# Optimization experiments

Measured on AMD Instinct MI355X. Metric: run time of the kernel, lower is better.

The kernel has to match this reference:

```python
import jax, jax.numpy as jnp
import numpy as np

B, LP, NC, D, E = 8, 1000, 64, 128, 320  # batch, protein len, compound atoms, hid dim, esm dim


def _linear_params(key, din, dout):
    k1, k2 = jax.random.split(key)
    lim = 1.0 / np.sqrt(din)
    W = jax.random.uniform(k1, (din, dout), minval=-lim, maxval=lim, dtype=jnp.float32)
    b = jax.random.uniform(k2, (dout,), minval=-lim, maxval=lim, dtype=jnp.float32)
    return W, b


def setup_inputs() -> dict:
    key = jax.random.key(0)
    ks = jax.random.split(key, 14)
    inp = {
        "protein_embedding": jax.random.normal(ks[0], (B, LP, E), dtype=jnp.float32),
        "protein_feat_x": jax.random.normal(ks[1], (B, LP, D), dtype=jnp.float32),
        "compound_feats": jax.random.normal(ks[2], (B, NC, D), dtype=jnp.float32),
    }
    layers = [("emb", E, D), ("wq", D, D), ("wk", D, D), ("wv", D, D), ("wo", D, D),
              ("jp", D, D), ("jc", D, D),
              ("c1", D, 1024), ("c2", 1024, 1024), ("c3", 1024, 256), ("c4", 256, 1)]
    for i, (name, din, dout) in enumerate(layers):
        W, b = _linear_params(ks[3 + i], din, dout)
        inp[name + "_w"] = W
        inp[name + "_b"] = b
    return inp


def reference(protein_embedding, protein_feat_x, compound_feats,
              emb_w, emb_b, wq_w, wq_b, wk_w, wk_b, wv_w, wv_b, wo_w, wo_b,
              jp_w, jp_b, jc_w, jc_b,
              c1_w, c1_b, c2_w, c2_b, c3_w, c3_b, c4_w, c4_b):
    # protein sequence embedding -> hid dim
    pe = protein_embedding @ emb_w + emb_b                      # [B, LP, D]
    # single-head cross attention: query = seq embedding, key/value = graph feats
    Q = pe @ wq_w + wq_b
    K = protein_feat_x @ wk_w + wk_b
    V = protein_feat_x @ wv_w + wv_b
    scale = jnp.sqrt(jnp.asarray(D, pe.dtype))                  # n_heads=1 -> head_dim=D
    attn = jax.nn.softmax(jnp.einsum('bqd,bkd->bqk', Q, K) / scale, axis=-1)
    protein_feats = jnp.einsum('bqk,bkd->bqd', attn, V) @ wo_w + wo_b  # [B, LP, D]

    # sigmoid bilinear joint attention over (protein residue, compound atom) pairs
    P = jax.nn.relu(protein_feats) @ jp_w + jp_b                # [B, LP, D]
    C = jax.nn.relu(compound_feats) @ jc_w + jc_b               # [B, NC, D]
    A = jax.nn.sigmoid(jnp.einsum('bid,bkd->bik', P, C))        # [B, LP, NC]
    A = A / jnp.sum(A, axis=(1, 2), keepdims=True)

    # tanh outer product (the costly 4D bikj intermediate) then weighted reduction
    cp = jnp.tanh(protein_feats[:, :, None, :] * compound_feats[:, None, :, :])  # [B, LP, NC, D]
    cp_embedding = jnp.einsum('bikd,bik->bd', cp, A)            # [B, D]

    # classifier MLP (dropout is eval-mode identity)
    h = jax.nn.relu(cp_embedding @ c1_w + c1_b)
    h = jax.nn.relu(h @ c2_w + c2_b)
    h = jax.nn.relu(h @ c3_w + c3_b)
    return h @ c4_w + c4_b                                      # [B, 1]
```

## Files before the change

kernel.cpp:

```cpp
#include <hip/hip_runtime.h>
#include <hip/hip_bf16.h>
#include <math.h>

#define LP 1000
#define NCMP 64
#define NSPLIT 4

typedef _Float16 f16;
typedef f16   v8h __attribute__((ext_vector_type(8)));
typedef float v4f __attribute__((ext_vector_type(4)));

__device__ __forceinline__ float rcp_fast(float x) { return __builtin_amdgcn_rcpf(x); }
__device__ __forceinline__ void fsplit(float x, f16& h, f16& l) {
    h = (f16)x; l = (f16)(x - (float)h);
}

__device__ __forceinline__ void gemm_core(float (*Ws)[128], float (*Xt)[36],
                                          const float* X, const float* W, const float* bias,
                                          float* Y, int K, int rowbase, bool relu_in)
{
    const int t  = threadIdx.x;
    const int r0 = (t >> 5) * 4;
    const int c0 = (t & 31) * 4;
    const int xr = t >> 3, xk = (t & 7) << 2;
    const int xrow = rowbase + xr;
    float4 xv = *(const float4*)(X + (long)xrow * K + xk);
    float4 wv[4];
    #pragma unroll
    for (int u = 0; u < 4; ++u) {
        int s = t + u * 256, r = s >> 5, cb = (s & 31) << 2;
        wv[u] = *(const float4*)(W + (long)r * 128 + cb);
    }
    float acc[4][4] = {};
    for (int k0 = 0; k0 < K; k0 += 32) {
        float4 xs = xv;
        if (relu_in) { xs.x = fmaxf(xs.x,0.f); xs.y = fmaxf(xs.y,0.f);
                       xs.z = fmaxf(xs.z,0.f); xs.w = fmaxf(xs.w,0.f); }
        Xt[xk+0][xr] = xs.x; Xt[xk+1][xr] = xs.y; Xt[xk+2][xr] = xs.z; Xt[xk+3][xr] = xs.w;
        #pragma unroll
        for (int u = 0; u < 4; ++u) {
            int s = t + u * 256, r = s >> 5, cb = (s & 31) << 2;
            *(float4*)&Ws[r][cb] = wv[u];
        }
        __syncthreads();
        if (k0 + 32 < K) {
            xv = *(const float4*)(X + (long)xrow * K + k0 + 32 + xk);
            #pragma unroll
            for (int u = 0; u < 4; ++u) {
                int s = t + u * 256, r = s >> 5, cb = (s & 31) << 2;
                wv[u] = *(const float4*)(W + (long)(k0 + 32 + r) * 128 + cb);
            }
        }
        #pragma unroll
        for (int kk = 0; kk < 32; ++kk) {
            float4 w4 = *(const float4*)&Ws[kk][c0];
            float4 x4 = *(const float4*)&Xt[kk][r0];
            acc[0][0] = fmaf(x4.x, w4.x, acc[0][0]); acc[0][1] = fmaf(x4.x, w4.y, acc[0][1]);
            acc[0][2] = fmaf(x4.x, w4.z, acc[0][2]); acc[0][3] = fmaf(x4.x, w4.w, acc[0][3]);
            acc[1][0] = fmaf(x4.y, w4.x, acc[1][0]); acc[1][1] = fmaf(x4.y, w4.y, acc[1][1]);
            acc[1][2] = fmaf(x4.y, w4.z, acc[1][2]); acc[1][3] = fmaf(x4.y, w4.w, acc[1][3]);
            acc[2][0] = fmaf(x4.z, w4.x, acc[2][0]); acc[2][1] = fmaf(x4.z, w4.y, acc[2][1]);
            acc[2][2] = fmaf(x4.z, w4.z, acc[2][2]); acc[2][3] = fmaf(x4.z, w4.w, acc[2][3]);
            acc[3][0] = fmaf(x4.w, w4.x, acc[3][0]); acc[3][1] = fmaf(x4.w, w4.y, acc[3][1]);
            acc[3][2] = fmaf(x4.w, w4.z, acc[3][2]); acc[3][3] = fmaf(x4.w, w4.w, acc[3][3]);
        }
        __syncthreads();
    }
    float4 bv = bias ? *(const float4*)(bias + c0) : make_float4(0.f,0.f,0.f,0.f);
    #pragma unroll
    for (int i = 0; i < 4; ++i) {
        int row = rowbase + r0 + i;
        float4 o;
        o.x = acc[i][0] + bv.x; o.y = acc[i][1] + bv.y;
        o.z = acc[i][2] + bv.z; o.w = acc[i][3] + bv.w;
        *(float4*)(Y + (long)row * 128 + c0) = o;
    }
}

struct H4 { f16 a, b, c, d; };

__device__ __forceinline__ void gemm_core16(float (*Ws)[128], float (*Xt)[36],
                                            const float* X, const float* W, const float* bias,
                                            f16* Yhi, f16* Ylo, int K, int rowbase)
{
    const int t  = threadIdx.x;
    const int r0 = (t >> 5) * 4;
    const int c0 = (t & 31) * 4;
    const int xr = t >> 3, xk = (t & 7) << 2;
    const int xrow = rowbase + xr;
    float4 xv = *(const float4*)(X + (long)xrow * K + xk);
    float4 wv[4];
    #pragma unroll
    for (int u = 0; u < 4; ++u) {
        int s = t + u * 256, r = s >> 5, cb = (s & 31) << 2;
        wv[u] = *(const float4*)(W + (long)r * 128 + cb);
    }
    float acc[4][4] = {};
    for (int k0 = 0; k0 < K; k0 += 32) {
        Xt[xk+0][xr] = xv.x; Xt[xk+1][xr] = xv.y; Xt[xk+2][xr] = xv.z; Xt[xk+3][xr] = xv.w;
        #pragma unroll
        for (int u = 0; u < 4; ++u) {
            int s = t + u * 256, r = s >> 5, cb = (s & 31) << 2;
            *(float4*)&Ws[r][cb] = wv[u];
        }
        __syncthreads();
        if (k0 + 32 < K) {
            xv = *(const float4*)(X + (long)xrow * K + k0 + 32 + xk);
            #pragma unroll
            for (int u = 0; u < 4; ++u) {
                int s = t + u * 256, r = s >> 5, cb = (s & 31) << 2;
                wv[u] = *(const float4*)(W + (long)(k0 + 32 + r) * 128 + cb);
            }
        }
        #pragma unroll
        for (int kk = 0; kk < 32; ++kk) {
            float4 w4 = *(const float4*)&Ws[kk][c0];
            float4 x4 = *(const float4*)&Xt[kk][r0];
            acc[0][0] = fmaf(x4.x, w4.x, acc[0][0]); acc[0][1] = fmaf(x4.x, w4.y, acc[0][1]);
            acc[0][2] = fmaf(x4.x, w4.z, acc[0][2]); acc[0][3] = fmaf(x4.x, w4.w, acc[0][3]);
            acc[1][0] = fmaf(x4.y, w4.x, acc[1][0]); acc[1][1] = fmaf(x4.y, w4.y, acc[1][1]);
            acc[1][2] = fmaf(x4.y, w4.z, acc[1][2]); acc[1][3] = fmaf(x4.y, w4.w, acc[1][3]);
            acc[2][0] = fmaf(x4.z, w4.x, acc[2][0]); acc[2][1] = fmaf(x4.z, w4.y, acc[2][1]);
            acc[2][2] = fmaf(x4.z, w4.z, acc[2][2]); acc[2][3] = fmaf(x4.z, w4.w, acc[2][3]);
            acc[3][0] = fmaf(x4.w, w4.x, acc[3][0]); acc[3][1] = fmaf(x4.w, w4.y, acc[3][1]);
            acc[3][2] = fmaf(x4.w, w4.z, acc[3][2]); acc[3][3] = fmaf(x4.w, w4.w, acc[3][3]);
        }
        __syncthreads();
    }
    float4 bv = *(const float4*)(bias + c0);
    #pragma unroll
    for (int i = 0; i < 4; ++i) {
        int row = rowbase + r0 + i;
        int bb = row / 1000, rr = row - bb * 1000;
        long base = ((long)bb * 1024 + rr) * 128 + c0;
        float o0 = acc[i][0]+bv.x, o1 = acc[i][1]+bv.y, o2 = acc[i][2]+bv.z, o3 = acc[i][3]+bv.w;
        H4 h, l;
        fsplit(o0, h.a, l.a); fsplit(o1, h.b, l.b); fsplit(o2, h.c, l.c); fsplit(o3, h.d, l.d);
        *(H4*)(Yhi + base) = h;
        *(H4*)(Ylo + base) = l;
    }
}

__global__ __launch_bounds__(256) void pre0_k(const float* __restrict__ emb_w, const float* __restrict__ emb_b,
                                              const float* __restrict__ wq_w, const float* __restrict__ wq_b,
                                              const float* __restrict__ wv_w, const float* __restrict__ wv_b,
                                              const float* __restrict__ wo_w, const float* __restrict__ wo_b,
                                              float* __restrict__ Wp, float* __restrict__ bp,
                                              float* __restrict__ Wvo, float* __restrict__ bvo,
                                              float* __restrict__ zbase)
{
    __shared__ __align__(16) float Ws[32][128];
    __shared__ __align__(16) float Xt[32][36];
    const int bid = blockIdx.x;
    if (bid < 10) { gemm_core(Ws, Xt, emb_w, wq_w, nullptr, Wp, 128, bid * 32, false); return; }
    if (bid >= 11 && bid < 15) { gemm_core(Ws, Xt, wv_w, wo_w, nullptr, Wvo, 128, (bid - 11) * 32, false); return; }
    int t = threadIdx.x;
    if (bid == 10 && t >= 128) {
        for (int i = t - 128; i < 1032; i += 128) zbase[i] = 0.f;
        return;
    }
    if (t < 128) {
        const float* vb = (bid == 10) ? emb_b : wv_b;
        const float* Wm = (bid == 10) ? wq_w  : wo_w;
        const float* ab = (bid == 10) ? wq_b  : wo_b;
        float a0 = 0.f, a1 = 0.f, a2 = 0.f, a3 = 0.f;
        for (int k = 0; k < 128; k += 4) {
            a0 = fmaf(vb[k+0], Wm[(k+0)*128 + t], a0);
            a1 = fmaf(vb[k+1], Wm[(k+1)*128 + t], a1);
            a2 = fmaf(vb[k+2], Wm[(k+2)*128 + t], a2);
            a3 = fmaf(vb[k+3], Wm[(k+3)*128 + t], a3);
        }
        float* dst = (bid == 10) ? bp : bvo;
        dst[t] = (a0 + a1) + (a2 + a3) + ab[t];
    }
}

__global__ __launch_bounds__(256) void qkv_k(const float* __restrict__ PE, const float* __restrict__ Wp,
                                             const float* __restrict__ bp, const float* __restrict__ PFX,
                                             const float* __restrict__ wk_w, const float* __restrict__ wk_b,
                                             const float* __restrict__ CF, const float* __restrict__ jc_w,
                                             const float* __restrict__ jc_b,
                                             f16* __restrict__ Qhi, f16* __restrict__ Qlo,
                                             f16* __restrict__ Khi, f16* __restrict__ Klo,
                                             f16* __restrict__ Vthi, f16* __restrict__ Vtlo,
                                             float* __restrict__ Cj)
{
    __shared__ __align__(16) float Ws[32][128];
    __shared__ __align__(16) float Xt[32][36];
    const int bid = blockIdx.x;
    if (bid < 250) { gemm_core16(Ws, Xt, PE, Wp, bp, Qhi, Qlo, 320, bid * 32); return; }
    if (bid < 500) { gemm_core16(Ws, Xt, PFX, wk_w, wk_b, Khi, Klo, 128, (bid - 250) * 32); return; }
    if (bid < 516) { gemm_core(Ws, Xt, CF, jc_w, jc_b, Cj, 128, (bid - 500) * 32, true); return; }
    const int t = threadIdx.x;
    const int rowbase = (bid - 516) * 32;
    const int d = t >> 1, half = t & 1;
    #pragma unroll 4
    for (int i = 0; i < 16; ++i) {
        int row = rowbase + half * 16 + i;
        int bb = row / 1000, rr = row - bb * 1000;
        float v = PFX[(long)row * 128 + d];
        f16 h, l; fsplit(v, h, l);
        long o = ((long)bb * 128 + d) * 1024 + rr;
        Vthi[o] = h; Vtlo[o] = l;
    }
}

__global__ __launch_bounds__(256) void flash7_k(const f16* __restrict__ Qhi, const f16* __restrict__ Qlo,
                                                const f16* __restrict__ Khi, const f16* __restrict__ Klo,
                                                const f16* __restrict__ Vthi, const f16* __restrict__ Vtlo,
                                                float* __restrict__ Opart,
                                                float* __restrict__ mpart, float* __restrict__ lpart)
{
    __shared__ __align__(16) f16 KVhi[9216];
    __shared__ __align__(16) f16 KVlo[9216];
    __shared__ __align__(16) f16 Pshi[4][16 * 72];
    __shared__ __align__(16) f16 Pslo[4][16 * 72];
    const int t    = threadIdx.x;
    const int wv   = t >> 6;
    const int lane = t & 63;
    const int quad = lane >> 4;
    const int l4   = lane & 15;
    const int qt = blockIdx.x, sp = blockIdx.y, b = blockIdx.z;
    const int q0 = qt * 64;
    const float SCALE = 0.08838834764831845f;
    const float L2E   = 1.4426950408889634f;

    int qrow = q0 + wv * 16 + l4; if (qrow >= LP) qrow = LP - 1;
    const long qbase = ((long)b * 1024 + qrow) * 128;
    v8h qh[4], ql[4];
    #pragma unroll
    for (int kt4 = 0; kt4 < 4; ++kt4) {
        qh[kt4] = *(const v8h*)(Qhi + qbase + kt4 * 32 + quad * 8);
        ql[kt4] = *(const v8h*)(Qlo + qbase + kt4 * 32 + quad * 8);
    }
    float m_i[4] = { -3.0e38f, -3.0e38f, -3.0e38f, -3.0e38f };
    float l_i[4] = { 0.f, 0.f, 0.f, 0.f };
    v4f  O[8];
    #pragma unroll
    for (int dt = 0; dt < 8; ++dt) O[dt] = (v4f){0.f, 0.f, 0.f, 0.f};

    for (int kt = sp * 4; kt < sp * 4 + 4; ++kt) {
        const int key0 = kt * 64;
        __syncthreads();
        #pragma unroll
        for (int u = 0; u < 4; ++u) {
            int ch = t + u * 256;
            int r = ch >> 4, co = (ch & 15) * 8;
            long ga = ((long)b * 1024 + key0 + r) * 128 + co;
            *(v8h*)(KVhi + r * 136 + co) = *(const v8h*)(Khi + ga);
            *(v8h*)(KVlo + r * 136 + co) = *(const v8h*)(Klo + ga);
        }
        __syncthreads();
        v8h vh[4], vl[4];
        #pragma unroll
        for (int u = 0; u < 4; ++u) {
            int ch = t + u * 256;
            int d = ch >> 3, co = (ch & 7) * 8;
            long ga = ((long)b * 128 + d) * 1024 + key0 + co;
            vh[u] = *(const v8h*)(Vthi + ga);
            vl[u] = *(const v8h*)(Vtlo + ga);
        }
        v4f S[4];
        #pragma unroll
        for (int nt = 0; nt < 4; ++nt) S[nt] = (v4f){0.f, 0.f, 0.f, 0.f};
        #pragma unroll
        for (int nt = 0; nt < 4; ++nt) {
            const int rb = (nt * 16 + l4) * 136;
            #pragma unroll
            for (int kt4 = 0; kt4 < 4; ++kt4) {
                v8h bh = *(const v8h*)(KVhi + rb + kt4 * 32 + quad * 8);
                v8h bl = *(const v8h*)(KVlo + rb + kt4 * 32 + quad * 8);
                S[nt] = __builtin_amdgcn_mfma_f32_16x16x32_f16(qh[kt4], bh, S[nt], 0, 0, 0);
                S[nt] = __builtin_amdgcn_mfma_f32_16x16x32_f16(qh[kt4], bl, S[nt], 0, 0, 0);
                S[nt] = __builtin_amdgcn_mfma_f32_16x16x32_f16(ql[kt4], bh, S[nt], 0, 0, 0);
            }
        }
        #pragma unroll
        for (int nt = 0; nt < 4; ++nt) {
            bool valid = (key0 + nt * 16 + l4) < LP;
            #pragma unroll
            for (int r = 0; r < 4; ++r)
                S[nt][r] = valid ? S[nt][r] * SCALE : -3.0e38f;
        }
        float alpha[4];
        #pragma unroll
        for (int r = 0; r < 4; ++r) {
            float tm = fmaxf(fmaxf(S[0][r], S[1][r]), fmaxf(S[2][r], S[3][r]));
            tm = fmaxf(tm, __shfl_xor(tm, 1));
            tm = fmaxf(tm, __shfl_xor(tm, 2));
            tm = fmaxf(tm, __shfl_xor(tm, 4));
            tm = fmaxf(tm, __shfl_xor(tm, 8));
            float mnew = fmaxf(m_i[r], tm);
            alpha[r] = exp2f((m_i[r] - mnew) * L2E);
            float ps = 0.f;
            #pragma unroll
            for (int nt = 0; nt < 4; ++nt) {
                float p = exp2f((S[nt][r] - mnew) * L2E);
                S[nt][r] = p;
                ps += p;
            }
            ps += __shfl_xor(ps, 1);
            ps += __shfl_xor(ps, 2);
            ps += __shfl_xor(ps, 4);
            ps += __shfl_xor(ps, 8);
            l_i[r] = l_i[r] * alpha[r] + ps;
            m_i[r] = mnew;
        }
        #pragma unroll
        for (int dt = 0; dt < 8; ++dt) {
            O[dt][0] *= alpha[0]; O[dt][1] *= alpha[1];
            O[dt][2] *= alpha[2]; O[dt][3] *= alpha[3];
        }
        __syncthreads();
        #pragma unroll
        for (int u = 0; u < 4; ++u) {
            int ch = t + u * 256;
            int d = ch >> 3, co = (ch & 7) * 8;
            *(v8h*)(KVhi + d * 72 + co) = vh[u];
            *(v8h*)(KVlo + d * 72 + co) = vl[u];
        }
        #pragma unroll
        for (int nt = 0; nt < 4; ++nt) {
            int col = nt * 16 + l4;
            #pragma unroll
            for (int r = 0; r < 4; ++r) {
                f16 ph, pl; fsplit(S[nt][r], ph, pl);
                Pshi[wv][(quad * 4 + r) * 72 + col] = ph;
                Pslo[wv][(quad * 4 + r) * 72 + col] = pl;
            }
        }
        __syncthreads();
        #pragma unroll
        for (int kc = 0; kc < 2; ++kc) {
            v8h pah = *(const v8h*)(Pshi[wv] + l4 * 72 + kc * 32 + quad * 8);
            v8h pal = *(const v8h*)(Pslo[wv] + l4 * 72 + kc * 32 + quad * 8);
            #pragma unroll
            for (int dt = 0; dt < 8; ++dt) {
                v8h vfh = *(const v8h*)(KVhi + (dt * 16 + l4) * 72 + kc * 32 + quad * 8);
                v8h vfl = *(const v8h*)(KVlo + (dt * 16 + l4) * 72 + kc * 32 + quad * 8);
                O[dt] = __builtin_amdgcn_mfma_f32_16x16x32_f16(pah, vfh, O[dt], 0, 0, 0);
                O[dt] = __builtin_amdgcn_mfma_f32_16x16x32_f16(pah, vfl, O[dt], 0, 0, 0);
                O[dt] = __builtin_amdgcn_mfma_f32_16x16x32_f16(pal, vfh, O[dt], 0, 0, 0);
            }
        }
    }
    #pragma unroll
    for (int r = 0; r < 4; ++r) {
        int row = q0 + wv * 16 + quad * 4 + r;
        if (row < LP) {
            long base = (long)sp * 1024000 + ((long)b * LP + row) * 128;
            #pragma unroll
            for (int dt = 0; dt < 8; ++dt)
                Opart[base + dt * 16 + l4] = O[dt][r];
            if (l4 == 0) {
                mpart[(long)sp * 8000 + b * LP + row] = m_i[r];
                lpart[(long)sp * 8000 + b * LP + row] = l_i[r];
            }
        }
    }
}

__global__ __launch_bounds__(256) void megatail_k(
    const float* __restrict__ Opart, const float* __restrict__ mp, const float* __restrict__ lp,
    const float* __restrict__ Wvo, const float* __restrict__ bvo,
    const float* __restrict__ jp_w, const float* __restrict__ jp_b,
    const float* __restrict__ Cj, const float* __restrict__ CF,
    float* __restrict__ Asum, float* __restrict__ cpe)
{
    __shared__ __align__(16) float WsA[32][132];
    __shared__ __align__(16) float Xt[32][20];
    __shared__ __align__(16) float AttS[16][132];
    __shared__ __align__(16) float Csh[64][132];
    __shared__ __align__(16) float Ash[16][64];
    __shared__ __align__(16) float AshT[64][20];
    __shared__ float red[256];
    const int t = threadIdx.x;
    const int p0 = blockIdx.x * 16;
    const int b  = blockIdx.y;
    const float L2E = 1.4426950408889634f;

    #pragma unroll
    for (int u = 0; u < 8; ++u) {
        int s = t + u * 256, r = s >> 5, cb = (s & 31) << 2;
        *(float4*)&Csh[r][cb] = *(const float4*)(Cj + ((long)b * NCMP + r) * 128 + cb);
    }
    const int r0 = (t >> 5) * 2, c0 = (t & 31) * 4;
    const int xr = t >> 3, xk = (t & 7) << 2;
    int prow = p0 + xr; if (prow > LP - 1) prow = LP - 1;
    const long g = (long)b * LP + prow;
    float wgt[NSPLIT]; float linv = 0.f;
    if (t < 128) {
        float mm = -3.0e38f;
        #pragma unroll
        for (int s = 0; s < NSPLIT; ++s) mm = fmaxf(mm, mp[g + (long)s * 8000]);
        float ls = 0.f;
        #pragma unroll
        for (int s = 0; s < NSPLIT; ++s) {
            wgt[s] = exp2f((mp[g + (long)s * 8000] - mm) * L2E);
            ls += wgt[s] * lp[g + (long)s * 8000];
        }
        linv = 1.0f / ls;
    }
    float4 xv = make_float4(0.f,0.f,0.f,0.f);
    float4 wv[4];
    if (t < 128) {
        float4 a = make_float4(0.f,0.f,0.f,0.f);
        #pragma unroll
        for (int s = 0; s < NSPLIT; ++s) {
            float4 p = *(const float4*)(Opart + (long)s * 1024000 + g * 128 + xk);
            a.x = fmaf(wgt[s], p.x, a.x); a.y = fmaf(wgt[s], p.y, a.y);
            a.z = fmaf(wgt[s], p.z, a.z); a.w = fmaf(wgt[s], p.w, a.w);
        }
        xv = make_float4(a.x * linv, a.y * linv, a.z * linv, a.w * linv);
    }
    #pragma unroll
    for (int u = 0; u < 4; ++u) {
        int s = t + u * 256, r = s >> 5, cb = (s & 31) << 2;
        wv[u] = *(const float4*)(Wvo + (long)r * 128 + cb);
    }
    float acc[2][4] = {};
    for (int k0 = 0; k0 < 128; k0 += 32) {
        if (t < 128) { Xt[xk+0][xr]=xv.x; Xt[xk+1][xr]=xv.y; Xt[xk+2][xr]=xv.z; Xt[xk+3][xr]=xv.w; }
        #pragma unroll
        for (int u = 0; u < 4; ++u) {
            int s = t + u * 256, r = s >> 5, cb = (s & 31) << 2;
            *(float4*)&WsA[r][cb] = wv[u];
        }
        __syncthreads();
        if (k0 + 32 < 128) {
            int kn = k0 + 32;
            if (t < 128) {
                float4 a = make_float4(0.f,0.f,0.f,0.f);
                #pragma unroll
                for (int s = 0; s < NSPLIT; ++s) {
                    float4 p = *(const float4*)(Opart + (long)s * 1024000 + g * 128 + kn + xk);
                    a.x = fmaf(wgt[s], p.x, a.x); a.y = fmaf(wgt[s], p.y, a.y);
                    a.z = fmaf(wgt[s], p.z, a.z); a.w = fmaf(wgt[s], p.w, a.w);
                }
                xv = make_float4(a.x * linv, a.y * linv, a.z * linv, a.w * linv);
            }
            #pragma unroll
            for (int u = 0; u < 4; ++u) {
                int s = t + u * 256, r = s >> 5, cb = (s & 31) << 2;
                wv[u] = *(const float4*)(Wvo + (long)(kn + r) * 128 + cb);
            }
        }
        #pragma unroll
        for (int kk = 0; kk < 32; ++kk) {
            float2 x2 = *(const float2*)&Xt[kk][r0];
            float4 w4 = *(const float4*)&WsA[kk][c0];
            acc[0][0]=fmaf(x2.x,w4.x,acc[0][0]); acc[0][1]=fmaf(x2.x,w4.y,acc[0][1]);
            acc[0][2]=fmaf(x2.x,w4.z,acc[0][2]); acc[0][3]=fmaf(x2.x,w4.w,acc[0][3]);
            acc[1][0]=fmaf(x2.y,w4.x,acc[1][0]); acc[1][1]=fmaf(x2.y,w4.y,acc[1][1]);
            acc[1][2]=fmaf(x2.y,w4.z,acc[1][2]); acc[1][3]=fmaf(x2.y,w4.w,acc[1][3]);
        }
        __syncthreads();
    }
    {
        float4 bv1 = *(const float4*)(bvo + c0);
        #pragma unroll
        for (int i = 0; i < 2; ++i)
            *(float4*)&AttS[r0 + i][c0] =
                make_float4(acc[i][0]+bv1.x, acc[i][1]+bv1.y, acc[i][2]+bv1.z, acc[i][3]+bv1.w);
    }
    float4 wv2[4];
    #pragma unroll
    for (int u = 0; u < 4; ++u) {
        int s = t + u * 256, r = s >> 5, cb = (s & 31) << 2;
        wv2[u] = *(const float4*)(jp_w + (long)r * 128 + cb);
    }
    float ac2[2][4] = {};
    for (int k0 = 0; k0 < 128; k0 += 32) {
        #pragma unroll
        for (int u = 0; u < 4; ++u) {
            int s = t + u * 256, r = s >> 5, cb = (s & 31) << 2;
            *(float4*)&WsA[r][cb] = wv2[u];
        }
        __syncthreads();
        if (k0 + 32 < 128) {
            #pragma unroll
            for (int u = 0; u < 4; ++u) {
                int s = t + u * 256, r = s >> 5, cb = (s & 31) << 2;
                wv2[u] = *(const float4*)(jp_w + (long)(k0 + 32 + r) * 128 + cb);
            }
        }
        #pragma unroll
        for (int kq = 0; kq < 8; ++kq) {
            float4 xa = *(const float4*)&AttS[r0 + 0][k0 + (kq << 2)];
            float4 xb = *(const float4*)&AttS[r0 + 1][k0 + (kq << 2)];
            #pragma unroll
            for (int e = 0; e < 4; ++e) {
                float x0 = fmaxf((e==0)?xa.x:(e==1)?xa.y:(e==2)?xa.z:xa.w, 0.f);
                float x1 = fmaxf((e==0)?xb.x:(e==1)?xb.y:(e==2)?xb.z:xb.w, 0.f);
                float4 w4 = *(const float4*)&WsA[(kq << 2) + e][c0];
                ac2[0][0]=fmaf(x0,w4.x,ac2[0][0]); ac2[0][1]=fmaf(x0,w4.y,ac2[0][1]);
                ac2[0][2]=fmaf(x0,w4.z,ac2[0][2]); ac2[0][3]=fmaf(x0,w4.w,ac2[0][3]);
                ac2[1][0]=fmaf(x1,w4.x,ac2[1][0]); ac2[1][1]=fmaf(x1,w4.y,ac2[1][1]);
                ac2[1][2]=fmaf(x1,w4.z,ac2[1][2]); ac2[1][3]=fmaf(x1,w4.w,ac2[1][3]);
            }
        }
        __syncthreads();
    }
    float (*Psh)[132] = WsA;
    {
        float4 b2 = *(const float4*)(jp_b + c0);
        #pragma unroll
        for (int i = 0; i < 2; ++i)
            *(float4*)&Psh[r0 + i][c0] =
                make_float4(ac2[i][0]+b2.x, ac2[i][1]+b2.y, ac2[i][2]+b2.z, ac2[i][3]+b2.w);
    }
    __syncthreads();
    const int tr = t >> 4, tc = t & 15;
    float sacc[4] = {};
    #pragma unroll 4
    for (int d4 = 0; d4 < 32; ++d4) {
        float4 p4 = *(const float4*)&Psh[tr][d4 << 2];
        #pragma unroll
        for (int j = 0; j < 4; ++j) {
            float4 cv = *(const float4*)&Csh[tc + (j << 4)][d4 << 2];
            sacc[j] += p4.x*cv.x + p4.y*cv.y + p4.z*cv.z + p4.w*cv.w;
        }
    }
    float lsum = 0.f;
    {
        int gi = p0 + tr;
        #pragma unroll
        for (int j = 0; j < 4; ++j) {
            float sg = rcp_fast(1.f + exp2f(-sacc[j] * L2E));
            if (gi < LP) {
                Ash[tr][tc + (j << 4)]  = sg;
                AshT[tc + (j << 4)][tr] = sg;
                lsum += sg;
            }
        }
    }
    red[t] = lsum;
    __syncthreads();
    for (int off = 128; off > 0; off >>= 1) {
        if (t < off) red[t] += red[t + off];
        __syncthreads();
    }
    if (t == 0) atomicAdd(Asum + b, red[0]);
    __syncthreads();
    #pragma unroll
    for (int u = 0; u < 8; ++u) {
        int s = t + u * 256, r = s >> 5, cb = (s & 31) << 2;
        *(float4*)&Csh[r][cb] = *(const float4*)(CF + ((long)b * NCMP + r) * 128 + cb);
    }
    __syncthreads();
    const float TWO_L2E = 2.8853900817779268f;
    const int d  = t & 127;
    const int kh = t >> 7;
    const int iiN = (LP - p0 < 16) ? (LP - p0) : 16;
    float areg[16];
    #pragma unroll
    for (int ii = 0; ii < 16; ++ii) areg[ii] = AttS[ii][d] * TWO_L2E;
    float accD = 0.f;
    for (int kk = 0; kk < 32; ++kk) {
        const int k = (kh << 5) + kk;
        const float cv = Csh[k][d];
        for (int iq = 0; iq < iiN; iq += 4) {
            float4 a4 = *(const float4*)&AshT[k][iq];
            float e0 = exp2f(areg[iq+0] * cv);
            float e1 = exp2f(areg[iq+1] * cv);
            float e2 = exp2f(areg[iq+2] * cv);
            float e3 = exp2f(areg[iq+3] * cv);
            accD = fmaf(1.f - 2.f * rcp_fast(e0 + 1.f), a4.x, accD);
            accD = fmaf(1.f - 2.f * rcp_fast(e1 + 1.f), a4.y, accD);
            accD = fmaf(1.f - 2.f * rcp_fast(e2 + 1.f), a4.z, accD);
            accD = fmaf(1.f - 2.f * rcp_fast(e3 + 1.f), a4.w, accD);
        }
    }
    red[t] = accD;
    __syncthreads();
    if (t < 128) atomicAdd(cpe + (long)b * 128 + t, red[t] + red[t + 128]);
}

__global__ __launch_bounds__(256) void c12_k(const float* __restrict__ cpe, const float* __restrict__ Asum,
                                             const float* __restrict__ c1_w, const float* __restrict__ c1_b,
                                             const float* __restrict__ c2_w, float* __restrict__ part)
{
    __shared__ float sc[8][128];
    __shared__ float ins[8][8];
    const int t = threadIdx.x, ks = blockIdx.x, k0 = ks * 8;
    #pragma unroll
    for (int u = 0; u < 4; ++u) {
        int idx = t + u * 256;
        sc[idx >> 7][idx & 127] = cpe[idx] * rcp_fast(Asum[idx >> 7]);
    }
    __syncthreads();
    if (t < 64) {
        int b = t >> 3, kk = t & 7;
        int n1 = k0 + kk;
        float a0 = 0.f, a1 = 0.f, a2 = 0.f, a3 = 0.f;
        #pragma unroll 8
        for (int j = 0; j < 128; j += 4) {
            a0 = fmaf(sc[b][j+0], c1_w[(long)(j+0)*1024 + n1], a0);
            a1 = fmaf(sc[b][j+1], c1_w[(long)(j+1)*1024 + n1], a1);
            a2 = fmaf(sc[b][j+2], c1_w[(long)(j+2)*1024 + n1], a2);
            a3 = fmaf(sc[b][j+3], c1_w[(long)(j+3)*1024 + n1], a3);
        }
        ins[b][kk] = fmaxf((a0 + a1) + (a2 + a3) + c1_b[n1], 0.f);
    }
    __syncthreads();
    const int n = (t & 63) * 4 + (t >> 6) * 256;
    float4 acc[8] = {};
    #pragma unroll
    for (int kk = 0; kk < 8; ++kk) {
        float4 w4 = *(const float4*)(c2_w + (long)(k0 + kk) * 1024 + n);
        #pragma unroll
        for (int b = 0; b < 8; ++b) {
            float s = ins[b][kk];
            acc[b].x = fmaf(s, w4.x, acc[b].x); acc[b].y = fmaf(s, w4.y, acc[b].y);
            acc[b].z = fmaf(s, w4.z, acc[b].z); acc[b].w = fmaf(s, w4.w, acc[b].w);
        }
    }
    #pragma unroll
    for (int b = 0; b < 8; ++b)
        *(float4*)(part + ((long)(ks * 8 + b)) * 1024 + n) = acc[b];
}

__global__ __launch_bounds__(256) void c3m_k(const float* __restrict__ part2, const float* __restrict__ c2_b,
                                             const float* __restrict__ c3_w, const float* __restrict__ c3_b,
                                             const float* __restrict__ c4_w, const float* __restrict__ c4_b,
                                             float* __restrict__ out)
{
    __shared__ float Hs[1024];
    __shared__ float red[256];
    const int t = threadIdx.x, b = blockIdx.x;
    float4 acc4 = make_float4(0.f,0.f,0.f,0.f);
    #pragma unroll 4
    for (int ks = 0; ks < 128; ++ks) {
        float4 p = *(const float4*)(part2 + ((long)(ks * 8 + b)) * 1024 + t * 4);
        acc4.x += p.x; acc4.y += p.y; acc4.z += p.z; acc4.w += p.w;
    }
    {
        float4 bb = *(const float4*)(c2_b + t * 4);
        Hs[t*4+0] = fmaxf(acc4.x + bb.x, 0.f);
        Hs[t*4+1] = fmaxf(acc4.y + bb.y, 0.f);
        Hs[t*4+2] = fmaxf(acc4.z + bb.z, 0.f);
        Hs[t*4+3] = fmaxf(acc4.w + bb.w, 0.f);
    }
    __syncthreads();
    float a0 = 0.f, a1 = 0.f, a2 = 0.f, a3 = 0.f;
    #pragma unroll 8
    for (int k = 0; k < 1024; k += 4) {
        a0 = fmaf(Hs[k+0], c3_w[(long)(k+0)*256 + t], a0);
        a1 = fmaf(Hs[k+1], c3_w[(long)(k+1)*256 + t], a1);
        a2 = fmaf(Hs[k+2], c3_w[(long)(k+2)*256 + t], a2);
        a3 = fmaf(Hs[k+3], c3_w[(long)(k+3)*256 + t], a3);
    }
    float h3v = fmaxf((a0 + a1) + (a2 + a3) + c3_b[t], 0.f);
    red[t] = h3v * c4_w[t];
    __syncthreads();
    for (int off = 128; off > 0; off >>= 1) {
        if (t < off) red[t] += red[t + off];
        __syncthreads();
    }
    if (t == 0) out[b] = red[0] + c4_b[0];
}

extern "C" void kernel_launch(void* const* d_in, const int* in_sizes, int n_in,
                              void* d_out, int out_size, void* d_ws, size_t ws_size,
                              hipStream_t stream)
{
    const float* PE   = (const float*)d_in[0];
    const float* PFX  = (const float*)d_in[1];
    const float* CF   = (const float*)d_in[2];
    const float* emb_w = (const float*)d_in[3];  const float* emb_b = (const float*)d_in[4];
    const float* wq_w  = (const float*)d_in[5];  const float* wq_b  = (const float*)d_in[6];
    const float* wk_w  = (const float*)d_in[7];  const float* wk_b  = (const float*)d_in[8];
    const float* wv_w  = (const float*)d_in[9];  const float* wv_b  = (const float*)d_in[10];
    const float* wo_w  = (const float*)d_in[11]; const float* wo_b  = (const float*)d_in[12];
    const float* jp_w  = (const float*)d_in[13]; const float* jp_b  = (const float*)d_in[14];
    const float* jc_w  = (const float*)d_in[15]; const float* jc_b  = (const float*)d_in[16];
    const float* c1_w  = (const float*)d_in[17]; const float* c1_b  = (const float*)d_in[18];
    const float* c2_w  = (const float*)d_in[19]; const float* c2_b  = (const float*)d_in[20];
    const float* c3_w  = (const float*)d_in[21]; const float* c3_b  = (const float*)d_in[22];
    const float* c4_w  = (const float*)d_in[23]; const float* c4_b  = (const float*)d_in[24];

    float* ws     = (float*)d_ws;
    f16*  Qhi   = (f16*)ws;
    f16*  Qlo   = (f16*)(ws + 524288);
    f16*  Khi   = (f16*)(ws + 1048576);
    f16*  Klo   = (f16*)(ws + 1572864);
    f16*  Vthi  = (f16*)(ws + 2097152);
    f16*  Vtlo  = (f16*)(ws + 2621440);
    float* bufC   = ws + 3145728;
    float* Opart  = bufC + 65536;
    float* mpart  = Opart + 4096000;
    float* lpart  = mpart + 32000;
    float* Asum   = lpart + 32000;
    float* cpe    = Asum + 8;
    float* bprime = cpe + 1024;
    float* bufWp  = bprime + 128;
    float* bufWvo = bufWp + 40960;
    float* bufbvo = bufWvo + 16384;
    float* part2  = ws;

    pre0_k<<<16, 256, 0, stream>>>(emb_w, emb_b, wq_w, wq_b, wv_w, wv_b, wo_w, wo_b,
                                   bufWp, bprime, bufWvo, bufbvo, Asum);
    qkv_k<<<766, 256, 0, stream>>>(PE, bufWp, bprime, PFX, wk_w, wk_b, CF, jc_w, jc_b,
                                   Qhi, Qlo, Khi, Klo, Vthi, Vtlo, bufC);
    flash7_k<<<dim3(16, NSPLIT, 8), 256, 0, stream>>>(Qhi, Qlo, Khi, Klo, Vthi, Vtlo,
                                                      Opart, mpart, lpart);
    megatail_k<<<dim3(63, 8), 256, 0, stream>>>(Opart, mpart, lpart, bufWvo, bufbvo,
                                                jp_w, jp_b, bufC, CF, Asum, cpe);
    c12_k<<<128, 256, 0, stream>>>(cpe, Asum, c1_w, c1_b, c2_w, part2);
    c3m_k<<<8, 256, 0, stream>>>(part2, c2_b, c3_w, c3_b, c4_w, c4_b, (float*)d_out);
}
```

Measured before the change: 278.8 us.

## Split megatail into projection kernel and compound-chunked tanh reduction kernel

```diff
diff --git a/kernel.cpp b/kernel.cpp
--- a/kernel.cpp
+++ b/kernel.cpp
@@ -360,30 +360,20 @@
     }
 }
 
-__global__ __launch_bounds__(256) void megatail_k(
+__global__ __launch_bounds__(256) void mt1_k(
     const float* __restrict__ Opart, const float* __restrict__ mp, const float* __restrict__ lp,
     const float* __restrict__ Wvo, const float* __restrict__ bvo,
     const float* __restrict__ jp_w, const float* __restrict__ jp_b,
-    const float* __restrict__ Cj, const float* __restrict__ CF,
-    float* __restrict__ Asum, float* __restrict__ cpe)
+    float* __restrict__ PF, float* __restrict__ PJ)
 {
     __shared__ __align__(16) float WsA[32][132];
     __shared__ __align__(16) float Xt[32][20];
     __shared__ __align__(16) float AttS[16][132];
-    __shared__ __align__(16) float Csh[64][132];
-    __shared__ __align__(16) float Ash[16][64];
-    __shared__ __align__(16) float AshT[64][20];
-    __shared__ float red[256];
     const int t = threadIdx.x;
     const int p0 = blockIdx.x * 16;
     const int b  = blockIdx.y;
     const float L2E = 1.4426950408889634f;
 
-    #pragma unroll
-    for (int u = 0; u < 8; ++u) {
-        int s = t + u * 256, r = s >> 5, cb = (s & 31) << 2;
-        *(float4*)&Csh[r][cb] = *(const float4*)(Cj + ((long)b * NCMP + r) * 128 + cb);
-    }
     const int r0 = (t >> 5) * 2, c0 = (t & 31) * 4;
     const int xr = t >> 3, xk = (t & 7) << 2;
     int prow = p0 + xr; if (prow > LP - 1) prow = LP - 1;
@@ -459,9 +449,12 @@
     {
         float4 bv1 = *(const float4*)(bvo + c0);
         #pragma unroll
-        for (int i = 0; i < 2; ++i)
-            *(float4*)&AttS[r0 + i][c0] =
-                make_float4(acc[i][0]+bv1.x, acc[i][1]+bv1.y, acc[i][2]+bv1.z, acc[i][3]+bv1.w);
+        for (int i = 0; i < 2; ++i) {
+            float4 o = make_float4(acc[i][0]+bv1.x, acc[i][1]+bv1.y, acc[i][2]+bv1.z, acc[i][3]+bv1.w);
+            *(float4*)&AttS[r0 + i][c0] = o;
+            int row = p0 + r0 + i;
+            if (row < LP) *(float4*)(PF + ((long)b * LP + row) * 128 + c0) = o;
+        }
     }
     float4 wv2[4];
     #pragma unroll
@@ -501,65 +494,28 @@
         }
         __syncthreads();
     }
-    float (*Psh)[132] = WsA;
     {
         float4 b2 = *(const float4*)(jp_b + c0);
         #pragma unroll
-        for (int i = 0; i < 2; ++i)
-            *(float4*)&Psh[r0 + i][c0] =
-                make_float4(ac2[i][0]+b2.x, ac2[i][1]+b2.y, ac2[i][2]+b2.z, ac2[i][3]+b2.w);
-    }
-    __syncthreads();
-    const int tr = t >> 4, tc = t & 15;
-    float sacc[4] = {};
-    #pragma unroll 4
-    for (int d4 = 0; d4 < 32; ++d4) {
-        float4 p4 = *(const float4*)&Psh[tr][d4 << 2];
-        #pragma unroll
-        for (int j = 0; j < 4; ++j) {
-            float4 cv = *(const float4*)&Csh[tc + (j << 4)][d4 << 2];
-            sacc[j] += p4.x*cv.x + p4.y*cv.y + p4.z*cv.z + p4.w*cv.w;
-        }
-    }
-    float lsum = 0.f;
-    {
-        int gi = p0 + tr;
-        #pragma unroll
-        for (int j = 0; j < 4; ++j) {
-            float sg = rcp_fast(1.f + exp2f(-sacc[j] * L2E));
-            if (gi < LP) {
-                Ash[tr][tc + (j << 4)]  = sg;
-                AshT[tc + (j << 4)][tr] = sg;
-                lsum += sg;
-            }
-        }
-    }
-    red[t] = lsum;
-    __syncthreads();
-    for (int off = 128; off > 0; off >>= 1) {
-        if (t < off) red[t] += red[t + off];
-        __syncthreads();
-    }
-    if (t == 0) atomicAdd(Asum + b, red[0]);
-    __syncthreads();
-    #pragma unroll
-    for (int u = 0; u < 8; ++u) {
-        int s = t + u * 256, r = s >> 5, cb = (s & 31) << 2;
-        *(float4*)&Csh[r][cb] = *(const float4*)(CF + ((long)b * NCMP + r) * 128 + cb);
-    }
-    __syncthreads();
-    const float TWO_L2E = 2.8853900817779268f;
-    const int d  = t & 127;
-    const int kh = t >> 7;
-    const int iiN = (LP - p0 < 16) ? (LP - p0) : 16;
-    float areg[16];
-    #pragma unroll
-    for (int ii = 0; ii < 16; ++ii) areg[ii] = AttS[ii][d] * TWO_L2E;
+        for (int i = 0; i < 2; ++i) {
+            int row = p0 + r0 + i;
+            if (row < LP)
+                *(float4*)(PJ + ((long)b * LP + row) * 128 + c0) =
+                    make_float4(ac2[i][0]+b2.x, ac2[i][1]+b2.y, ac2[i][2]+b2.z, ac2[i][3]+b2.w);
+        }
+    }
+}
+
+template<int IIN>
+__device__ __forceinline__ float tanh_chunk(const float (*Cs)[132], const float (*AshT)[20],
+                                            const float* areg, int d, int kh)
+{
     float accD = 0.f;
-    for (int kk = 0; kk < 32; ++kk) {
-        const int k = (kh << 5) + kk;
-        const float cv = Csh[k][d];
-        for (int iq = 0; iq < iiN; iq += 4) {
+    for (int kk = 0; kk < 16; ++kk) {
+        const int k = (kh << 4) + kk;
+        const float cv = Cs[k][d];
+        #pragma unroll
+        for (int iq = 0; iq < IIN; iq += 4) {
             float4 a4 = *(const float4*)&AshT[k][iq];
             float e0 = exp2f(areg[iq+0] * cv);
             float e1 = exp2f(areg[iq+1] * cv);
@@ -571,6 +527,78 @@
             accD = fmaf(1.f - 2.f * rcp_fast(e3 + 1.f), a4.w, accD);
         }
     }
+    return accD;
+}
+
+__global__ __launch_bounds__(256) void mt2_k(
+    const float* __restrict__ PF, const float* __restrict__ PJ,
+    const float* __restrict__ Cj, const float* __restrict__ CF,
+    float* __restrict__ Asum, float* __restrict__ cpe)
+{
+    __shared__ __align__(16) float Pjs[16][132];
+    __shared__ __align__(16) float Pfs[16][132];
+    __shared__ __align__(16) float Cs[32][132];
+    __shared__ __align__(16) float AshT[32][20];
+    __shared__ float red[256];
+    const int t  = threadIdx.x;
+    const int p0 = blockIdx.x * 16;
+    const int kc = blockIdx.y;
+    const int b  = blockIdx.z;
+    const float L2E = 1.4426950408889634f;
+
+    {
+        int pr = t >> 4, pc = (t & 15) << 3;
+        int gr = p0 + pr; if (gr > LP - 1) gr = LP - 1;
+        long gb = ((long)b * LP + gr) * 128 + pc;
+        *(float4*)&Pjs[pr][pc]     = *(const float4*)(PJ + gb);
+        *(float4*)&Pjs[pr][pc + 4] = *(const float4*)(PJ + gb + 4);
+        *(float4*)&Pfs[pr][pc]     = *(const float4*)(PF + gb);
+        *(float4*)&Pfs[pr][pc + 4] = *(const float4*)(PF + gb + 4);
+    }
+    float4 cfv[4];
+    #pragma unroll
+    for (int u = 0; u < 4; ++u) {
+        int s = t + u * 256, r = s >> 5, cb = (s & 31) << 2;
+        *(float4*)&Cs[r][cb] = *(const float4*)(Cj + ((long)b * NCMP + kc * 32 + r) * 128 + cb);
+        cfv[u] = *(const float4*)(CF + ((long)b * NCMP + kc * 32 + r) * 128 + cb);
+    }
+    __syncthreads();
+    const int tr = t >> 4, tc = t & 15;
+    float sacc[2] = {0.f, 0.f};
+    #pragma unroll 4
+    for (int d4 = 0; d4 < 32; ++d4) {
+        float4 p4 = *(const float4*)&Pjs[tr][d4 << 2];
+        #pragma unroll
+        for (int j = 0; j < 2; ++j) {
+            float4 cv = *(const float4*)&Cs[tc + (j << 4)][d4 << 2];
+            sacc[j] += p4.x*cv.x + p4.y*cv.y + p4.z*cv.z + p4.w*cv.w;
+        }
+    }
+    float lsum = 0.f;
+    const int gi = p0 + tr;
+    #pragma unroll
+    for (int j = 0; j < 2; ++j) {
+        float sg = rcp_fast(1.f + exp2f(-sacc[j] * L2E));
+        if (gi < LP) { AshT[tc + (j << 4)][tr] = sg; lsum += sg; }
+    }
+    #pragma unroll
+    for (int off = 1; off < 64; off <<= 1) lsum += __shfl_xor(lsum, off);
+    if ((t & 63) == 0) red[t >> 6] = lsum;
+    __syncthreads();
+    if (t == 0) atomicAdd(Asum + b, (red[0] + red[1]) + (red[2] + red[3]));
+    #pragma unroll
+    for (int u = 0; u < 4; ++u) {
+        int s = t + u * 256, r = s >> 5, cb = (s & 31) << 2;
+        *(float4*)&Cs[r][cb] = cfv[u];
+    }
+    __syncthreads();
+    const float TWO_L2E = 2.8853900817779268f;
+    const int d = t & 127, kh = t >> 7;
+    float areg[16];
+    #pragma unroll
+    for (int ii = 0; ii < 16; ++ii) areg[ii] = Pfs[ii][d] * TWO_L2E;
+    float accD = (p0 + 16 <= LP) ? tanh_chunk<16>(Cs, AshT, areg, d, kh)
+                                 : tanh_chunk<8>(Cs, AshT, areg, d, kh);
     red[t] = accD;
     __syncthreads();
     if (t < 128) atomicAdd(cpe + (long)b * 128 + t, red[t] + red[t + 128]);
@@ -697,6 +725,8 @@
     float* bufWvo = bufWp + 40960;
     float* bufbvo = bufWvo + 16384;
     float* part2  = ws;
+    float* PFbuf  = ws + 1048576;
+    float* PJbuf  = ws + 2097152;
 
     pre0_k<<<16, 256, 0, stream>>>(emb_w, emb_b, wq_w, wq_b, wv_w, wv_b, wo_w, wo_b,
                                    bufWp, bprime, bufWvo, bufbvo, Asum);
@@ -704,8 +734,9 @@
                                    Qhi, Qlo, Khi, Klo, Vthi, Vtlo, bufC);
     flash7_k<<<dim3(16, NSPLIT, 8), 256, 0, stream>>>(Qhi, Qlo, Khi, Klo, Vthi, Vtlo,
                                                       Opart, mpart, lpart);
-    megatail_k<<<dim3(63, 8), 256, 0, stream>>>(Opart, mpart, lpart, bufWvo, bufbvo,
-                                                jp_w, jp_b, bufC, CF, Asum, cpe);
+    mt1_k<<<dim3(63, 8), 256, 0, stream>>>(Opart, mpart, lpart, bufWvo, bufbvo,
+                                           jp_w, jp_b, PFbuf, PJbuf);
+    mt2_k<<<dim3(63, 2, 8), 256, 0, stream>>>(PFbuf, PJbuf, bufC, CF, Asum, cpe);
     c12_k<<<128, 256, 0, stream>>>(cpe, Asum, c1_w, c1_b, c2_w, part2);
     c3m_k<<<8, 256, 0, stream>>>(part2, c2_b, c3_w, c3_b, c4_w, c4_b, (float*)d_out);
 }
```

After: 287.8 us. 3.2% more time.
